# Performance work log

Measured on AMD Instinct MI355X. Metric: run time of the kernel, lower is better.

Reference implementation:

```python
import jax, jax.numpy as jnp
import numpy as np

N, E = 50000, 800000
IN, H1, H2, HEADS, EMB = 128, 32, 32, 4, 128
NEG_SLOPE = 0.2  # DGL GATConv default leaky_relu slope


def setup_inputs() -> dict:
    key = jax.random.key(0)
    ks = jax.random.split(key, 14)
    s = 0.05
    return {
        "x": jax.random.normal(ks[0], (N, IN), jnp.float32),
        "src": jax.random.randint(ks[1], (E,), 0, N, jnp.int32),
        "dst": jax.random.randint(ks[2], (E,), 0, N, jnp.int32),
        "W1": jax.random.normal(ks[3], (IN, HEADS * H1), jnp.float32) * s,
        "al1": jax.random.normal(ks[4], (HEADS, H1), jnp.float32) * s,
        "ar1": jax.random.normal(ks[5], (HEADS, H1), jnp.float32) * s,
        "b1": jnp.zeros((HEADS * H1,), jnp.float32),
        "W2": jax.random.normal(ks[6], (HEADS * H1, HEADS * H2), jnp.float32) * s,
        "al2": jax.random.normal(ks[7], (HEADS, H2), jnp.float32) * s,
        "ar2": jax.random.normal(ks[8], (HEADS, H2), jnp.float32) * s,
        "b2": jnp.zeros((HEADS * H2,), jnp.float32),
        "Wp": jax.random.normal(ks[9], (HEADS * H2, EMB), jnp.float32) * s,
        "bp": jnp.zeros((EMB,), jnp.float32),
    }


def gat_layer(x, W, al, ar, b, src, dst, heads, d_out):
    n = x.shape[0]
    feat = (x @ W).reshape(n, heads, d_out)            # [N,H,D]
    el = (feat * al).sum(-1)                           # [N,H]
    er = (feat * ar).sum(-1)                           # [N,H]
    e = jax.nn.leaky_relu(el[src] + er[dst], NEG_SLOPE)  # [E,H]
    # edge softmax over destination segments
    m = jax.ops.segment_max(e, dst, num_segments=n)    # [N,H] (-inf for empty)
    ex = jnp.exp(e - m[dst])                           # [E,H]
    z = jax.ops.segment_sum(ex, dst, num_segments=n)   # [N,H]
    alpha = ex / z[dst]                                # [E,H]
    msg = alpha[:, :, None] * feat[src]                # [E,H,D]
    out = jax.ops.segment_sum(msg, dst, num_segments=n)  # [N,H,D]
    return out + b.reshape(1, heads, d_out)


def reference(x, src, dst, W1, al1, ar1, b1, W2, al2, ar2, b2, Wp, bp):
    h = gat_layer(x, W1, al1, ar1, b1, src, dst, HEADS, H1).reshape(N, -1)
    h = gat_layer(h, W2, al2, ar2, b2, src, dst, HEADS, H2).reshape(N, -1)
    out = h @ Wp + bp
    return (h, out)
```

## Files before the change

kernel.cpp:

```cpp
#include <hip/hip_runtime.h>
#include <hip/hip_bf16.h>

#define N_NODES 50000
#define HEADS 4
#define DHEAD 32
#define F 128
#define NEG_SLOPE 0.2f

typedef unsigned int uint;
typedef unsigned short ushort;
typedef __attribute__((ext_vector_type(8))) short bf16x8;
typedef __attribute__((ext_vector_type(4))) float f32x4;

__device__ __forceinline__ float bf2f(ushort u) {
    union { uint i; float f; } c; c.i = ((uint)u) << 16; return c.f;
}
__device__ __forceinline__ ushort f2bf(float f) {
    union { float f; uint i; } c; c.f = f;
    uint u = c.i + 0x7FFF + ((c.i >> 16) & 1);
    return (ushort)(u >> 16);
}
__device__ __forceinline__ float sel4(int h, float a, float b, float c, float d) {
    return (h & 2) ? ((h & 1) ? d : c) : ((h & 1) ? b : a);
}

__global__ void rank_hist_kernel(const int* __restrict__ dst, int* __restrict__ counts,
                                 int* __restrict__ rank, int E) {
    int i = blockIdx.x * 256 + threadIdx.x;
    if (i < E) rank[i] = atomicAdd(&counts[dst[i]], 1);
}

__global__ __launch_bounds__(256) void scanA_kernel(const int* __restrict__ counts,
                                                    int* __restrict__ local_sc,
                                                    int* __restrict__ partials, int N) {
    int i = blockIdx.x * 256 + threadIdx.x;
    int v = (i < N) ? counts[i] : 0;
    int lane = threadIdx.x & 63;
    int w = threadIdx.x >> 6;
    int x = v;
#pragma unroll
    for (int off = 1; off < 64; off <<= 1) {
        int t = __shfl_up(x, off);
        if (lane >= off) x += t;
    }
    __shared__ int wsum[4];
    if (lane == 63) wsum[w] = x;
    __syncthreads();
    int wpre = 0;
#pragma unroll
    for (int k = 0; k < 4; k++)
        if (k < w) wpre += wsum[k];
    if (i < N) local_sc[i] = x - v + wpre;
    if (threadIdx.x == 255) partials[blockIdx.x] = wpre + x;
}

__global__ void scanB_kernel(int* __restrict__ partials, int NP) {
    int tid = threadIdx.x;
    int v = (tid < NP) ? partials[tid] : 0;
    int lane = tid & 63;
    int w = tid >> 6;
    int x = v;
#pragma unroll
    for (int off = 1; off < 64; off <<= 1) {
        int t = __shfl_up(x, off);
        if (lane >= off) x += t;
    }
    __shared__ int wsum[4];
    if (lane == 63) wsum[w] = x;
    __syncthreads();
    int wpre = 0;
#pragma unroll
    for (int k = 0; k < 4; k++)
        if (k < w) wpre += wsum[k];
    if (tid < NP) partials[tid] = x - v + wpre;
}

__global__ __launch_bounds__(256) void scanC_kernel(int* __restrict__ offs,
                                                    const int* __restrict__ partials,
                                                    int N, int E) {
    int i = blockIdx.x * 256 + threadIdx.x;
    if (i < N) offs[i] += partials[blockIdx.x];
    if (i == 0) offs[N] = E;
}

#define SCH 2048
__global__ __launch_bounds__(256) void scatter_ranged_kernel(
    const int* __restrict__ src, const int* __restrict__ dst,
    const int* __restrict__ rank, const int* __restrict__ offs,
    int* __restrict__ csr_src, int E) {
    int range = blockIdx.x & 7;
    int chunk = blockIdx.x >> 3;
    int base = chunk * SCH + threadIdx.x;
    int lo = (int)(((long long)range * E) >> 3);
    int hi = (int)(((long long)(range + 1) * E) >> 3);
#pragma unroll
    for (int k = 0; k < SCH / 256; k++) {
        int i = base + k * 256;
        if (i < E) {
            int p = offs[dst[i]] + rank[i];
            if (p >= lo && p < hi) csr_src[p] = src[i];
        }
    }
}

__global__ __launch_bounds__(256) void wtrans_kernel(const float* __restrict__ W1,
                                                     const float* __restrict__ W2,
                                                     const float* __restrict__ Wp,
                                                     ushort* __restrict__ WT) {
    const float* W = (blockIdx.x == 0) ? W1 : (blockIdx.x == 1) ? W2 : Wp;
    ushort* T = WT + (size_t)blockIdx.x * 128 * 128;
    for (int i = threadIdx.x; i < 128 * 128; i += 256) {
        int r = i >> 7, c = i & 127;
        T[c * 128 + r] = f2bf(W[i]);
    }
}

template <bool A_FP32, bool OUT_BF16, bool BIAS, bool ELER>
__global__ __launch_bounds__(256) void mfma_gemm_kernel(
    const void* __restrict__ Av, const ushort* __restrict__ BT,
    const float* __restrict__ bias,
    const float* __restrict__ al, const float* __restrict__ ar,
    void* __restrict__ Cv, float* __restrict__ el, float* __restrict__ er, int M) {
    int wid = threadIdx.x >> 6;
    int lane = threadIdx.x & 63;
    int row0 = blockIdx.x * 64 + wid * 16;
    int rsub = lane & 15;
    int kg = lane >> 4;
    int row = row0 + rsub;
    int rowc = (row < M) ? row : (M - 1);

    bf16x8 af[4];
    if (A_FP32) {
        const float* A = (const float*)Av;
        const float* ap = A + (size_t)rowc * 128 + kg * 8;
#pragma unroll
        for (int ks = 0; ks < 4; ks++) {
            float4 lo = *(const float4*)(ap + ks * 32);
            float4 hi = *(const float4*)(ap + ks * 32 + 4);
            bf16x8 v;
            v[0] = (short)f2bf(lo.x); v[1] = (short)f2bf(lo.y);
            v[2] = (short)f2bf(lo.z); v[3] = (short)f2bf(lo.w);
            v[4] = (short)f2bf(hi.x); v[5] = (short)f2bf(hi.y);
            v[6] = (short)f2bf(hi.z); v[7] = (short)f2bf(hi.w);
            af[ks] = v;
        }
    } else {
        const ushort* A = (const ushort*)Av;
        const ushort* ap = A + (size_t)rowc * 128 + kg * 8;
#pragma unroll
        for (int ks = 0; ks < 4; ks++) af[ks] = *(const bf16x8*)(ap + ks * 32);
    }

    f32x4 acc[8];
#pragma unroll
    for (int ct = 0; ct < 8; ct++) acc[ct] = (f32x4){0.f, 0.f, 0.f, 0.f};

    const ushort* bp = BT + (size_t)rsub * 128 + kg * 8;
#pragma unroll
    for (int ks = 0; ks < 4; ks++) {
#pragma unroll
        for (int ct = 0; ct < 8; ct++) {
            bf16x8 bf = *(const bf16x8*)(bp + (size_t)ct * 16 * 128 + ks * 32);
            acc[ct] = __builtin_amdgcn_mfma_f32_16x16x32_bf16(af[ks], bf, acc[ct], 0, 0, 0);
        }
    }

    if (row0 >= M) return;

#pragma unroll
    for (int ct = 0; ct < 8; ct++) {
        int col = ct * 16 + rsub;
        float bv = BIAS ? bias[col] : 0.f;
#pragma unroll
        for (int r = 0; r < 4; r++) {
            int gr = row0 + kg * 4 + r;
            if (gr < M) {
                float v = acc[ct][r] + bv;
                if (OUT_BF16) ((ushort*)Cv)[(size_t)gr * 128 + col] = f2bf(v);
                else          ((float*)Cv)[(size_t)gr * 128 + col] = v;
            }
        }
    }

    if (ELER) {
        float alv[8], arv[8];
#pragma unroll
        for (int ct = 0; ct < 8; ct++) {
            alv[ct] = al[ct * 16 + rsub];
            arv[ct] = ar[ct * 16 + rsub];
        }
        float pl[4][4], pr[4][4];
#pragma unroll
        for (int r = 0; r < 4; r++)
#pragma unroll
            for (int hh = 0; hh < 4; hh++) {
                pl[r][hh] = acc[2 * hh][r] * alv[2 * hh] + acc[2 * hh + 1][r] * alv[2 * hh + 1];
                pr[r][hh] = acc[2 * hh][r] * arv[2 * hh] + acc[2 * hh + 1][r] * arv[2 * hh + 1];
            }
#pragma unroll
        for (int off = 1; off < 16; off <<= 1) {
#pragma unroll
            for (int r = 0; r < 4; r++)
#pragma unroll
                for (int hh = 0; hh < 4; hh++) {
                    pl[r][hh] += __shfl_xor(pl[r][hh], off);
                    pr[r][hh] += __shfl_xor(pr[r][hh], off);
                }
        }
        if (rsub < 4) {
#pragma unroll
            for (int r = 0; r < 4; r++) {
                int gr = row0 + kg * 4 + r;
                if (gr < M) {
                    el[(size_t)gr * 4 + rsub] = pl[r][rsub];
                    er[(size_t)gr * 4 + rsub] = pr[r][rsub];
                }
            }
        }
    }
}

template <bool F32OUT>
__global__ __launch_bounds__(256) void aggregate_kernel(
    const ushort* __restrict__ featb, const float* __restrict__ el,
    const float* __restrict__ er, const float* __restrict__ bias,
    const int* __restrict__ offsets, const int* __restrict__ csr_src,
    void* __restrict__ outv, int N) {
    int tid = threadIdx.x;
    int gl = tid & 15;
    int lane = tid & 63;
    int n = blockIdx.x * 16 + (tid >> 4);
    if (n >= N) return;
    int start = offsets[n], end = offsets[n + 1];

    float4 erv = *(const float4*)(er + (size_t)n * 4);
    float er_h[4] = {erv.x, erv.y, erv.z, erv.w};

    float m[4], s[4];
#pragma unroll
    for (int h = 0; h < 4; h++) { m[h] = -1e30f; s[h] = 0.f; }

    for (int e = start + gl; e < end; e += 16) {
        int sv = csr_src[e];
        float4 ev = *(const float4*)(el + (size_t)sv * 4);
        float elh[4] = {ev.x, ev.y, ev.z, ev.w};
#pragma unroll
        for (int h = 0; h < 4; h++) {
            float v = elh[h] + er_h[h];
            v = (v >= 0.f) ? v : NEG_SLOPE * v;
            float mn = fmaxf(m[h], v);
            s[h] = s[h] * __expf(m[h] - mn) + __expf(v - mn);
            m[h] = mn;
        }
    }
#pragma unroll
    for (int off = 1; off < 16; off <<= 1) {
#pragma unroll
        for (int h = 0; h < 4; h++) {
            float mo = __shfl_xor(m[h], off);
            float so = __shfl_xor(s[h], off);
            float mn = fmaxf(m[h], mo);
            s[h] = s[h] * __expf(m[h] - mn) + so * __expf(mo - mn);
            m[h] = mn;
        }
    }

    int h0 = gl >> 2;
    int j  = gl & 3;
    int c0 = gl * 8;
    float mh  = sel4(h0, m[0], m[1], m[2], m[3]);
    float sh  = sel4(h0, s[0], s[1], s[2], s[3]);
    float erh = sel4(h0, er_h[0], er_h[1], er_h[2], er_h[3]);
    float rzh = (end > start) ? 1.0f / sh : 0.f;
    int bidx = lane & 60;

    float acc[8] = {};
    for (int e = start; e < end; e += 4) {
        int rem = end - e;
        int ej = e + ((j < rem) ? j : 0);
        int svj = csr_src[ej];
        float v = el[(size_t)svj * 4 + h0] + erh;
        v = (v >= 0.f) ? v : NEG_SLOPE * v;
        float a = __expf(v - mh) * rzh;
        if (j >= rem) a = 0.f;
#pragma unroll
        for (int jj = 0; jj < 4; jj++) {
            float ajj = __shfl(a, bidx | jj);
            int svjj  = __shfl(svj, bidx | jj);
            uint4 f0 = *(const uint4*)(featb + (size_t)svjj * 128 + c0);
            acc[0] = fmaf(ajj, bf2f(f0.x & 0xFFFF), acc[0]);
            acc[1] = fmaf(ajj, bf2f(f0.x >> 16),    acc[1]);
            acc[2] = fmaf(ajj, bf2f(f0.y & 0xFFFF), acc[2]);
            acc[3] = fmaf(ajj, bf2f(f0.y >> 16),    acc[3]);
            acc[4] = fmaf(ajj, bf2f(f0.z & 0xFFFF), acc[4]);
            acc[5] = fmaf(ajj, bf2f(f0.z >> 16),    acc[5]);
            acc[6] = fmaf(ajj, bf2f(f0.w & 0xFFFF), acc[6]);
            acc[7] = fmaf(ajj, bf2f(f0.w >> 16),    acc[7]);
        }
    }

    float4 b0 = *(const float4*)(bias + c0);
    float4 b1 = *(const float4*)(bias + c0 + 4);
    float o[8];
    o[0] = acc[0] + b0.x; o[1] = acc[1] + b0.y; o[2] = acc[2] + b0.z; o[3] = acc[3] + b0.w;
    o[4] = acc[4] + b1.x; o[5] = acc[5] + b1.y; o[6] = acc[6] + b1.z; o[7] = acc[7] + b1.w;
    if (F32OUT) {
        float* outf = (float*)outv;
        float4 w0, w1;
        w0.x = o[0]; w0.y = o[1]; w0.z = o[2]; w0.w = o[3];
        w1.x = o[4]; w1.y = o[5]; w1.z = o[6]; w1.w = o[7];
        *(float4*)(outf + (size_t)n * 128 + c0) = w0;
        *(float4*)(outf + (size_t)n * 128 + c0 + 4) = w1;
    } else {
        ushort* outb = (ushort*)outv;
        uint4 p;
        p.x = (uint)f2bf(o[0]) | ((uint)f2bf(o[1]) << 16);
        p.y = (uint)f2bf(o[2]) | ((uint)f2bf(o[3]) << 16);
        p.z = (uint)f2bf(o[4]) | ((uint)f2bf(o[5]) << 16);
        p.w = (uint)f2bf(o[6]) | ((uint)f2bf(o[7]) << 16);
        *(uint4*)(outb + (size_t)n * 128 + c0) = p;
    }
}

extern "C" void kernel_launch(void* const* d_in, const int* in_sizes, int n_in,
                              void* d_out, int out_size, void* d_ws, size_t ws_size,
                              hipStream_t stream) {
    const float* x   = (const float*)d_in[0];
    const int*   src = (const int*)d_in[1];
    const int*   dst = (const int*)d_in[2];
    const float* W1  = (const float*)d_in[3];
    const float* al1 = (const float*)d_in[4];
    const float* ar1 = (const float*)d_in[5];
    const float* b1  = (const float*)d_in[6];
    const float* W2  = (const float*)d_in[7];
    const float* al2 = (const float*)d_in[8];
    const float* ar2 = (const float*)d_in[9];
    const float* b2  = (const float*)d_in[10];
    const float* Wp  = (const float*)d_in[11];
    const float* bp  = (const float*)d_in[12];

    const int N = in_sizes[0] / F;
    const int E = in_sizes[1];

    float* h_out = (float*)d_out;
    float* p_out = h_out + (size_t)N * F;

    char* w = (char*)d_ws;
    ushort* featb   = (ushort*)w;
    ushort* h1b     = featb + (size_t)N * F;
    float* el       = (float*)(h1b + (size_t)N * F);
    float* er       = el + (size_t)N * 4;
    int*   offs     = (int*)(er + (size_t)N * 4);
    int*   counts   = offs + (N + 1);
    int*   rank     = counts + N;
    int*   csrsrc   = rank + E;
    int*   partials = csrsrc + E;
    ushort* WT      = (ushort*)(partials + 256);

    const int NB = (N + 255) / 256;
    const int EB = (E + 255) / 256;

    hipMemsetAsync(counts, 0, (size_t)N * 4, stream);
    rank_hist_kernel<<<EB, 256, 0, stream>>>(dst, counts, rank, E);
    scanA_kernel<<<NB, 256, 0, stream>>>(counts, offs, partials, N);
    scanB_kernel<<<1, 256, 0, stream>>>(partials, NB);
    scanC_kernel<<<NB, 256, 0, stream>>>(offs, partials, N, E);
    scatter_ranged_kernel<<<8 * ((E + SCH - 1) / SCH), 256, 0, stream>>>(
        src, dst, rank, offs, csrsrc, E);

    wtrans_kernel<<<3, 256, 0, stream>>>(W1, W2, Wp, WT);
    ushort* WT1 = WT;
    ushort* WT2 = WT + 128 * 128;
    ushort* WTp = WT + 2 * 128 * 128;

    int ggrid = (N + 63) / 64;
    int agrid = (N + 15) / 16;

    mfma_gemm_kernel<true, true, false, true><<<ggrid, 256, 0, stream>>>(
        x, WT1, nullptr, al1, ar1, featb, el, er, N);
    aggregate_kernel<false><<<agrid, 256, 0, stream>>>(featb, el, er, b1, offs, csrsrc, h1b, N);

    mfma_gemm_kernel<false, true, false, true><<<ggrid, 256, 0, stream>>>(
        h1b, WT2, nullptr, al2, ar2, featb, el, er, N);
    aggregate_kernel<true><<<agrid, 256, 0, stream>>>(featb, el, er, b2, offs, csrsrc, h_out, N);

    mfma_gemm_kernel<true, false, true, false><<<ggrid, 256, 0, stream>>>(
        h_out, WTp, bp, nullptr, nullptr, p_out, nullptr, nullptr, N);
}
```

Baseline: 262.6 us.

## Degree-sort aggregation nodes, fold attention vectors into GEMM, precompute edge positions

```diff
diff --git a/kernel.cpp b/kernel.cpp
--- a/kernel.cpp
+++ b/kernel.cpp
@@ -32,9 +32,11 @@
 
 __global__ __launch_bounds__(256) void scanA_kernel(const int* __restrict__ counts,
                                                     int* __restrict__ local_sc,
-                                                    int* __restrict__ partials, int N) {
+                                                    int* __restrict__ partials,
+                                                    int* __restrict__ degbin, int N) {
     int i = blockIdx.x * 256 + threadIdx.x;
     int v = (i < N) ? counts[i] : 0;
+    if (i < N) atomicAdd(&degbin[v < 63 ? v : 63], 1);
     int lane = threadIdx.x & 63;
     int w = threadIdx.x >> 6;
     int x = v;
@@ -54,7 +56,8 @@
     if (threadIdx.x == 255) partials[blockIdx.x] = wpre + x;
 }
 
-__global__ void scanB_kernel(int* __restrict__ partials, int NP) {
+__global__ void scanB_kernel(int* __restrict__ partials, int NP,
+                             int* __restrict__ degbin, int* __restrict__ degcur) {
     int tid = threadIdx.x;
     int v = (tid < NP) ? partials[tid] : 0;
     int lane = tid & 63;
@@ -73,20 +76,43 @@
     for (int k = 0; k < 4; k++)
         if (k < w) wpre += wsum[k];
     if (tid < NP) partials[tid] = x - v + wpre;
+    if (tid < 64) {
+        int dv = degbin[tid];
+        int dx = dv;
+#pragma unroll
+        for (int off = 1; off < 64; off <<= 1) {
+            int t = __shfl_up(dx, off);
+            if (lane >= off) dx += t;
+        }
+        degcur[tid] = dx - dv;
+    }
 }
 
 __global__ __launch_bounds__(256) void scanC_kernel(int* __restrict__ offs,
                                                     const int* __restrict__ partials,
+                                                    const int* __restrict__ counts,
+                                                    int* __restrict__ degcur,
+                                                    int* __restrict__ perm,
                                                     int N, int E) {
     int i = blockIdx.x * 256 + threadIdx.x;
-    if (i < N) offs[i] += partials[blockIdx.x];
+    if (i < N) {
+        offs[i] += partials[blockIdx.x];
+        int d = counts[i];
+        int pos = atomicAdd(&degcur[d < 63 ? d : 63], 1);
+        perm[pos] = i;
+    }
     if (i == 0) offs[N] = E;
+}
+
+__global__ void posfix_kernel(const int* __restrict__ dst, const int* __restrict__ offs,
+                              int* __restrict__ rank, int E) {
+    int i = blockIdx.x * 256 + threadIdx.x;
+    if (i < E) rank[i] += offs[dst[i]];
 }
 
 #define SCH 2048
 __global__ __launch_bounds__(256) void scatter_ranged_kernel(
-    const int* __restrict__ src, const int* __restrict__ dst,
-    const int* __restrict__ rank, const int* __restrict__ offs,
+    const int* __restrict__ src, const int* __restrict__ pos,
     int* __restrict__ csr_src, int E) {
     int range = blockIdx.x & 7;
     int chunk = blockIdx.x >> 3;
@@ -97,29 +123,49 @@
     for (int k = 0; k < SCH / 256; k++) {
         int i = base + k * 256;
         if (i < E) {
-            int p = offs[dst[i]] + rank[i];
+            int p = pos[i];
             if (p >= lo && p < hi) csr_src[p] = src[i];
         }
     }
 }
 
-__global__ __launch_bounds__(256) void wtrans_kernel(const float* __restrict__ W1,
-                                                     const float* __restrict__ W2,
-                                                     const float* __restrict__ Wp,
-                                                     ushort* __restrict__ WT) {
-    const float* W = (blockIdx.x == 0) ? W1 : (blockIdx.x == 1) ? W2 : Wp;
-    ushort* T = WT + (size_t)blockIdx.x * 128 * 128;
-    for (int i = threadIdx.x; i < 128 * 128; i += 256) {
-        int r = i >> 7, c = i & 127;
-        T[c * 128 + r] = f2bf(W[i]);
+__global__ __launch_bounds__(256) void wtrans_kernel(
+    const float* __restrict__ W1, const float* __restrict__ W2,
+    const float* __restrict__ Wp,
+    const float* __restrict__ al1, const float* __restrict__ ar1,
+    const float* __restrict__ al2, const float* __restrict__ ar2,
+    ushort* __restrict__ WT) {
+    if (blockIdx.x < 3) {
+        const float* W = (blockIdx.x == 0) ? W1 : (blockIdx.x == 1) ? W2 : Wp;
+        ushort* T = WT + (size_t)blockIdx.x * 128 * 128;
+        for (int i = threadIdx.x; i < 128 * 128; i += 256) {
+            int r = i >> 7, c = i & 127;
+            T[c * 128 + r] = f2bf(W[i]);
+        }
+    } else {
+        const float* W   = (blockIdx.x == 3) ? W1 : W2;
+        const float* a_l = (blockIdx.x == 3) ? al1 : al2;
+        const float* a_r = (blockIdx.x == 3) ? ar1 : ar2;
+        ushort* T = WT + 3 * 128 * 128 + (blockIdx.x - 3) * 16 * 128;
+        for (int i = threadIdx.x; i < 16 * 128; i += 256) {
+            int c = i >> 7, k = i & 127;
+            float v = 0.f;
+            if (c < 8) {
+                int h = c & 3;
+                const float* a  = (c < 4) ? (a_l + h * 32) : (a_r + h * 32);
+                const float* wr = W + k * 128 + h * 32;
+#pragma unroll
+                for (int d = 0; d < 32; d++) v += wr[d] * a[d];
+            }
+            T[i] = f2bf(v);
+        }
     }
 }
 
 template <bool A_FP32, bool OUT_BF16, bool BIAS, bool ELER>
 __global__ __launch_bounds__(256) void mfma_gemm_kernel(
     const void* __restrict__ Av, const ushort* __restrict__ BT,
-    const float* __restrict__ bias,
-    const float* __restrict__ al, const float* __restrict__ ar,
+    const float* __restrict__ bias, const ushort* __restrict__ ALR,
     void* __restrict__ Cv, float* __restrict__ el, float* __restrict__ er, int M) {
     int wid = threadIdx.x >> 6;
     int lane = threadIdx.x & 63;
@@ -165,6 +211,16 @@
         }
     }
 
+    f32x4 acce = (f32x4){0.f, 0.f, 0.f, 0.f};
+    if (ELER) {
+        const ushort* ep = ALR + rsub * 128 + kg * 8;
+#pragma unroll
+        for (int ks = 0; ks < 4; ks++) {
+            bf16x8 eb = *(const bf16x8*)(ep + ks * 32);
+            acce = __builtin_amdgcn_mfma_f32_16x16x32_bf16(af[ks], eb, acce, 0, 0, 0);
+        }
+    }
+
     if (row0 >= M) return;
 
 #pragma unroll
@@ -182,39 +238,13 @@
         }
     }
 
-    if (ELER) {
-        float alv[8], arv[8];
-#pragma unroll
-        for (int ct = 0; ct < 8; ct++) {
-            alv[ct] = al[ct * 16 + rsub];
-            arv[ct] = ar[ct * 16 + rsub];
-        }
-        float pl[4][4], pr[4][4];
-#pragma unroll
-        for (int r = 0; r < 4; r++)
-#pragma unroll
-            for (int hh = 0; hh < 4; hh++) {
-                pl[r][hh] = acc[2 * hh][r] * alv[2 * hh] + acc[2 * hh + 1][r] * alv[2 * hh + 1];
-                pr[r][hh] = acc[2 * hh][r] * arv[2 * hh] + acc[2 * hh + 1][r] * arv[2 * hh + 1];
-            }
-#pragma unroll
-        for (int off = 1; off < 16; off <<= 1) {
-#pragma unroll
-            for (int r = 0; r < 4; r++)
-#pragma unroll
-                for (int hh = 0; hh < 4; hh++) {
-                    pl[r][hh] += __shfl_xor(pl[r][hh], off);
-                    pr[r][hh] += __shfl_xor(pr[r][hh], off);
-                }
-        }
-        if (rsub < 4) {
-#pragma unroll
-            for (int r = 0; r < 4; r++) {
-                int gr = row0 + kg * 4 + r;
-                if (gr < M) {
-                    el[(size_t)gr * 4 + rsub] = pl[r][rsub];
-                    er[(size_t)gr * 4 + rsub] = pr[r][rsub];
-                }
+    if (ELER && rsub < 8) {
+#pragma unroll
+        for (int r = 0; r < 4; r++) {
+            int gr = row0 + kg * 4 + r;
+            if (gr < M) {
+                if (rsub < 4) el[(size_t)gr * 4 + rsub] = acce[r];
+                else          er[(size_t)gr * 4 + (rsub - 4)] = acce[r];
             }
         }
     }
@@ -225,12 +255,13 @@
     const ushort* __restrict__ featb, const float* __restrict__ el,
     const float* __restrict__ er, const float* __restrict__ bias,
     const int* __restrict__ offsets, const int* __restrict__ csr_src,
-    void* __restrict__ outv, int N) {
+    const int* __restrict__ perm, void* __restrict__ outv, int N) {
     int tid = threadIdx.x;
     int gl = tid & 15;
     int lane = tid & 63;
-    int n = blockIdx.x * 16 + (tid >> 4);
-    if (n >= N) return;
+    int slot = blockIdx.x * 16 + (tid >> 4);
+    if (slot >= N) return;
+    int n = perm[slot];
     int start = offsets[n], end = offsets[n + 1];
 
     float4 erv = *(const float4*)(er + (size_t)n * 4);
@@ -352,7 +383,10 @@
     float* er       = el + (size_t)N * 4;
     int*   offs     = (int*)(er + (size_t)N * 4);
     int*   counts   = offs + (N + 1);
-    int*   rank     = counts + N;
+    int*   degbin   = counts + N;
+    int*   degcur   = degbin + 64;
+    int*   perm     = degcur + 64;
+    int*   rank     = perm + N;
     int*   csrsrc   = rank + E;
     int*   partials = csrsrc + E;
     ushort* WT      = (ushort*)(partials + 256);
@@ -360,30 +394,34 @@
     const int NB = (N + 255) / 256;
     const int EB = (E + 255) / 256;
 
-    hipMemsetAsync(counts, 0, (size_t)N * 4, stream);
+    hipMemsetAsync(counts, 0, (size_t)(N + 64) * 4, stream);
     rank_hist_kernel<<<EB, 256, 0, stream>>>(dst, counts, rank, E);
-    scanA_kernel<<<NB, 256, 0, stream>>>(counts, offs, partials, N);
-    scanB_kernel<<<1, 256, 0, stream>>>(partials, NB);
-    scanC_kernel<<<NB, 256, 0, stream>>>(offs, partials, N, E);
-    scatter_ranged_kernel<<<8 * ((E + SCH - 1) / SCH), 256, 0, stream>>>(
-        src, dst, rank, offs, csrsrc, E);
-
-    wtrans_kernel<<<3, 256, 0, stream>>>(W1, W2, Wp, WT);
-    ushort* WT1 = WT;
-    ushort* WT2 = WT + 128 * 128;
-    ushort* WTp = WT + 2 * 128 * 128;
+    scanA_kernel<<<NB, 256, 0, stream>>>(counts, offs, partials, degbin, N);
+    scanB_kernel<<<1, 256, 0, stream>>>(partials, NB, degbin, degcur);
+    scanC_kernel<<<NB, 256, 0, stream>>>(offs, partials, counts, degcur, perm, N, E);
+    posfix_kernel<<<EB, 256, 0, stream>>>(dst, offs, rank, E);
+    scatter_ranged_kernel<<<8 * ((E + SCH - 1) / SCH), 256, 0, stream>>>(src, rank, csrsrc, E);
+
+    wtrans_kernel<<<5, 256, 0, stream>>>(W1, W2, Wp, al1, ar1, al2, ar2, WT);
+    ushort* WT1  = WT;
+    ushort* WT2  = WT + 128 * 128;
+    ushort* WTp  = WT + 2 * 128 * 128;
+    ushort* ALR1 = WT + 3 * 128 * 128;
+    ushort* ALR2 = ALR1 + 16 * 128;
 
     int ggrid = (N + 63) / 64;
     int agrid = (N + 15) / 16;
 
     mfma_gemm_kernel<true, true, false, true><<<ggrid, 256, 0, stream>>>(
-        x, WT1, nullptr, al1, ar1, featb, el, er, N);
-    aggregate_kernel<false><<<agrid, 256, 0, stream>>>(featb, el, er, b1, offs, csrsrc, h1b, N);
+        x, WT1, nullptr, ALR1, featb, el, er, N);
+    aggregate_kernel<false><<<agrid, 256, 0, stream>>>(
+        featb, el, er, b1, offs, csrsrc, perm, h1b, N);
 
     mfma_gemm_kernel<false, true, false, true><<<ggrid, 256, 0, stream>>>(
-        h1b, WT2, nullptr, al2, ar2, featb, el, er, N);
-    aggregate_kernel<true><<<agrid, 256, 0, stream>>>(featb, el, er, b2, offs, csrsrc, h_out, N);
+        h1b, WT2, nullptr, ALR2, featb, el, er, N);
+    aggregate_kernel<true><<<agrid, 256, 0, stream>>>(
+        featb, el, er, b2, offs, csrsrc, perm, h_out, N);
 
     mfma_gemm_kernel<true, false, true, false><<<ggrid, 256, 0, stream>>>(
-        h_out, WTp, bp, nullptr, nullptr, p_out, nullptr, nullptr, N);
-}
+        h_out, WTp, bp, nullptr, p_out, nullptr, nullptr, N);
+}
```

Result: slower. 516.7 us (+96.8%).
